# Performance work log

Hardware: AMD Instinct MI355X
Metric: run time of the kernel (lower is better)

The kernel has to match this reference:

```python
import jax, jax.numpy as jnp
import numpy as np
import math

SCALES = (1, 2, 4)
GROUPS = 8
EPS = 1e-5
TEMPERATURE = 1.0


def bilinear_resize(x, out_h, out_w):
    # torch F.interpolate mode='bilinear', align_corners=False
    B, C, h, w = x.shape
    def coords(out, in_):
        c = (jnp.arange(out, dtype=x.dtype) + 0.5) * (in_ / out) - 0.5
        c = jnp.clip(c, 0.0, in_ - 1.0)
        i0 = jnp.floor(c).astype(jnp.int32)
        i1 = jnp.minimum(i0 + 1, in_ - 1)
        t = c - i0.astype(x.dtype)
        return i0, i1, t
    y0, y1, ty = coords(out_h, h)
    x0, x1, tx = coords(out_w, w)
    r0 = x[:, :, y0, :]
    r1 = x[:, :, y1, :]
    v00 = r0[:, :, :, x0]; v01 = r0[:, :, :, x1]
    v10 = r1[:, :, :, x0]; v11 = r1[:, :, :, x1]
    top = v00 * (1.0 - tx) + v01 * tx
    bot = v10 * (1.0 - tx) + v11 * tx
    return top * (1.0 - ty)[:, None] + bot * ty[:, None]


def group_norm(x, gamma, beta):
    B, C, H, W = x.shape
    xg = x.reshape(B, GROUPS, C // GROUPS, H, W)
    mu = xg.mean(axis=(2, 3, 4), keepdims=True)
    var = xg.var(axis=(2, 3, 4), keepdims=True)
    xn = ((xg - mu) * jax.lax.rsqrt(var + EPS)).reshape(B, C, H, W)
    return xn * gamma[None, :, None, None] + beta[None, :, None, None]


def setup_inputs() -> dict:
    key = jax.random.key(0)
    B, C, H, W = 4, 128, 64, 64
    inter = max(C // 4, 8)  # 32
    S = len(SCALES)
    ks = jax.random.split(key, 8)
    def xavier(k, shape, fan_in, fan_out):
        a = math.sqrt(6.0 / (fan_in + fan_out))
        return jax.random.uniform(k, shape, jnp.float32, -a, a)
    inp = {
        'x': jax.random.normal(ks[0], (B, C, H, W), jnp.float32),
        'gn_w': jnp.ones((S, C), jnp.float32),
        'gn_b': jnp.zeros((S, C), jnp.float32),
        'qw': xavier(ks[1], (S, inter, C), C, inter),
        'qb': jnp.zeros((S, inter), jnp.float32),
        'kw': xavier(ks[2], (S, inter, C), C, inter),
        'kb': jnp.zeros((S, inter), jnp.float32),
        'vw': xavier(ks[3], (S, inter, C), C, inter),
        'vb': jnp.zeros((S, inter), jnp.float32),
        'ow': xavier(ks[4], (S, C, inter), inter, C),
        'ob': jnp.zeros((S, C), jnp.float32),
        'gamma': jnp.full((S,), 0.1 / S, jnp.float32),
        'scale_weights': jnp.full((S,), 1.0 / S, jnp.float32),
    }
    return inp


def _forward(x, gn_w, gn_b, qw, qb, kw, kb, vw, vb, ow, ob, gamma, scale_weights):
    B, C, H, W = x.shape
    inter = qw.shape[1]
    inv_scale = 1.0 / (TEMPERATURE * math.sqrt(inter))
    outs = []
    for i, s in enumerate(SCALES):
        if s == 1:
            xs = x
        else:
            xs = x.reshape(B, C, H // s, s, W // s, s).mean(axis=(3, 5))
        h, w = xs.shape[2], xs.shape[3]
        N = h * w
        xn = group_norm(xs, gn_w[i], gn_b[i])
        # 1x1 convs as channel contractions
        q = (jnp.einsum('oc,bchw->bohw', qw[i], xn) + qb[i][None, :, None, None]).reshape(B, inter, N)
        k = (jnp.einsum('oc,bchw->bohw', kw[i], xn) + kb[i][None, :, None, None]).reshape(B, inter, N)
        v = (jnp.einsum('oc,bchw->bohw', vw[i], xn) + vb[i][None, :, None, None]).reshape(B, inter, N)
        logits = jnp.einsum('bin,bim->bnm', q, k) * inv_scale  # [B, N, N]
        attn = jax.nn.softmax(logits, axis=-1)
        att = jnp.einsum('bnm,bim->bin', attn, v).reshape(B, inter, h, w)
        o = jnp.einsum('ci,bihw->bchw', ow[i], att) + ob[i][None, :, None, None]
        y = gamma[i] * o + xs
        if s > 1:
            y = bilinear_resize(y, H, W)
        outs.append(y)
    wts = jax.nn.softmax(scale_weights, axis=0)
    fused = wts[0] * outs[0]
    for i in range(1, len(outs)):
        fused = fused + wts[i] * outs[i]
    return fused


def reference(x, gn_w, gn_b, qw, qb, kw, kb, vw, vb, ow, ob, gamma, scale_weights):
    return _forward(x, gn_w, gn_b, qw, qb, kw, kb, vw, vb, ow, ob, gamma, scale_weights)
```

## Files before the change

kernel.cpp:

```cpp
#include <hip/hip_runtime.h>
#include <math.h>

#define B 4
#define C 128
#define CPG 16
#define INTER 32
#define SPLIT 16
#define KS1 8
#define KS24 4

#define N1 4096
#define N2 1024
#define N4 256

#define QOFF2 (B * N1 * 32)
#define QOFF4 (QOFF2 + B * N2 * 32)
#define QTOT  (QOFF4 + B * N4 * 32)
#define PAOFF2 (B * KS1 * 32 * N1)
#define PAOFF4 (PAOFF2 + B * KS24 * 32 * N2)
#define PATOT  (PAOFF4 + B * KS24 * 32 * N4)
#define PMOFF2 (B * KS1 * 2 * N1)
#define PMOFF4 (PMOFF2 + B * KS24 * 2 * N2)
#define PMTOT  (PMOFF4 + B * KS24 * 2 * N4)

#define QSCALE 0.25503490f

typedef unsigned short ushort_t;
typedef __attribute__((ext_vector_type(8))) short short8;
typedef __attribute__((ext_vector_type(4))) float f32x4;

__device__ __forceinline__ ushort_t f2bf(float f) {
    union { float f; unsigned u; } x; x.f = f;
    unsigned r = x.u + 0x7fffu + ((x.u >> 16) & 1u);
    return (ushort_t)(r >> 16);
}

__device__ __forceinline__ void scale_wts(const float* __restrict__ sw,
                                          float& w0, float& w1, float& w2) {
    float a = sw[0], b = sw[1], c = sw[2];
    float m = fmaxf(a, fmaxf(b, c));
    float e0 = __expf(a - m), e1 = __expf(b - m), e2 = __expf(c - m);
    float inv = 1.0f / (e0 + e1 + e2);
    w0 = e0 * inv; w1 = e1 * inv; w2 = e2 * inv;
}

__device__ __forceinline__ void block_reduce_write(float s, float q,
                                                   float* __restrict__ dst2) {
    __shared__ float rs[256], rq[256];
    rs[threadIdx.x] = s; rq[threadIdx.x] = q;
    __syncthreads();
    for (int st = 128; st > 0; st >>= 1) {
        if (threadIdx.x < st) {
            rs[threadIdx.x] += rs[threadIdx.x + st];
            rq[threadIdx.x] += rq[threadIdx.x + st];
        }
        __syncthreads();
    }
    if (threadIdx.x == 0) { dst2[0] = rs[0]; dst2[1] = rq[0]; }
}

__global__ __launch_bounds__(256) void pool_stats_kernel(const float* __restrict__ x,
                                                         float* __restrict__ xs2,
                                                         float* __restrict__ xs4,
                                                         float* __restrict__ part) {
    int bid = blockIdx.x;
    if (bid < 512) {
        int sp = bid & 15, bg = bid >> 4;
        const float* base = x + ((bg * CPG) << 12) + sp * 4096;
        float s = 0.0f, q = 0.0f;
        for (int i = threadIdx.x; i < 4096; i += 256) {
            float v = base[i];
            s += v; q += v * v;
        }
        block_reduce_write(s, q, part + bid * 2);
    } else if (bid < 1024) {
        int blk = bid - 512;
        int sp = blk & 15, bg = blk >> 4;
        int bc = bg * CPG + sp;
        const float* src = x + (bc << 12);
        float* dst = xs2 + (bc << 10);
        float s = 0.0f, q = 0.0f;
        for (int p = threadIdx.x; p < 1024; p += 256) {
            int oy = p >> 5, ox = p & 31;
            const float* s2 = src + oy * 128 + ox * 2;
            float v = (s2[0] + s2[1] + s2[64] + s2[65]) * 0.25f;
            dst[p] = v; s += v; q += v * v;
        }
        block_reduce_write(s, q, part + 1024 + blk * 2);
    } else {
        int blk = bid - 1024;
        int sp = blk & 15, bg = blk >> 4;
        int bc = bg * CPG + sp;
        const float* src = x + (bc << 12);
        float* dst = xs4 + (bc << 8);
        int p = threadIdx.x & 255;
        int oy = p >> 4, ox = p & 15;
        const float* s4 = src + oy * 256 + ox * 4;
        float v = 0.0f;
        #pragma unroll
        for (int dy = 0; dy < 4; ++dy)
            #pragma unroll
            for (int dx = 0; dx < 4; ++dx) v += s4[dy * 64 + dx];
        v *= 0.0625f;
        dst[p] = v;
        block_reduce_write(v, v * v, part + 2048 + blk * 2);
    }
}

template <int N, int NSH>
__device__ __forceinline__ void qkv_body(int bi, const float* __restrict__ xs,
    const float* __restrict__ part,
    const float* __restrict__ gn_w, const float* __restrict__ gn_b,
    const float* __restrict__ qw, const float* __restrict__ qb,
    const float* __restrict__ kw, const float* __restrict__ kb,
    const float* __restrict__ vw, const float* __restrict__ vb,
    ushort_t* __restrict__ q_bf, ushort_t* __restrict__ k_bf, ushort_t* __restrict__ v_bf) {
    const int nc = N >> 8;
    int nchunk = bi % nc; bi /= nc;
    int og = bi & 3; bi >>= 2;
    int proj = bi % 3; int b = bi / 3;
    const float* wp = (proj == 0) ? qw : ((proj == 1) ? kw : vw);
    const float* bp = (proj == 0) ? qb : ((proj == 1) ? kb : vb);
    __shared__ float wl[8 * 128];
    __shared__ float2 ss[128];
    {
        int t = threadIdx.x;
        #pragma unroll
        for (int r = 0; r < 4; ++r) {
            int e = r * 256 + t;
            int o = e >> 7, c0 = e & 127;
            wl[c0 * 8 + o] = wp[(og * 8 + o) * C + c0];
        }
        if (t < 128) {
            int c = t;
            int bg = b * 8 + (c >> 4);
            float s = 0.0f, q = 0.0f;
            #pragma unroll
            for (int sp = 0; sp < SPLIT; ++sp) {
                s += part[(bg * SPLIT + sp) * 2];
                q += part[(bg * SPLIT + sp) * 2 + 1];
            }
            float inv = 1.0f / (float)(CPG << NSH);
            float mu = s * inv;
            float var = q * inv - mu * mu;
            float a = rsqrtf(var + 1e-5f) * gn_w[c];
            float2 r; r.x = a; r.y = gn_b[c] - mu * a;
            ss[c] = r;
        }
    }
    __syncthreads();
    int n = nchunk * 256 + threadIdx.x;
    const float* xb = xs + ((size_t)(b * C) << NSH) + n;
    float acc[8];
    #pragma unroll
    for (int o = 0; o < 8; ++o) acc[o] = bp[og * 8 + o];
    #pragma unroll 2
    for (int c0 = 0; c0 < C; ++c0) {
        float raw = xb[(size_t)c0 << NSH];
        float2 s2 = ss[c0];
        float xv = fmaf(s2.x, raw, s2.y);
        const float4* wr = (const float4*)&wl[c0 * 8];
        float4 w0 = wr[0], w1 = wr[1];
        acc[0] += w0.x * xv; acc[1] += w0.y * xv; acc[2] += w0.z * xv; acc[3] += w0.w * xv;
        acc[4] += w1.x * xv; acc[5] += w1.y * xv; acc[6] += w1.z * xv; acc[7] += w1.w * xv;
    }
    if (proj < 2) {
        float fs = (proj == 0) ? QSCALE : 1.0f;
        ushort_t tmp[8];
        #pragma unroll
        for (int o = 0; o < 8; ++o) tmp[o] = f2bf(acc[o] * fs);
        ushort_t* dst = ((proj == 0) ? q_bf : k_bf) + ((size_t)(b * N + n)) * 32 + og * 8;
        *(uint4*)dst = *(const uint4*)tmp;
    } else {
        #pragma unroll
        for (int o = 0; o < 8; ++o)
            v_bf[((size_t)(b * 32 + og * 8 + o) << NSH) + n] = f2bf(acc[o]);
    }
}

__global__ __launch_bounds__(256) void qkv_all_kernel(const float* __restrict__ x,
    const float* __restrict__ xs2, const float* __restrict__ xs4,
    const float* __restrict__ part,
    const float* __restrict__ gn_w, const float* __restrict__ gn_b,
    const float* __restrict__ qw, const float* __restrict__ qb,
    const float* __restrict__ kw, const float* __restrict__ kb,
    const float* __restrict__ vw, const float* __restrict__ vb,
    ushort_t* __restrict__ qbf, ushort_t* __restrict__ kbf, ushort_t* __restrict__ vbf) {
    int bid = blockIdx.x;
    if (bid < 768) {
        qkv_body<N1, 12>(bid, x, part, gn_w, gn_b, qw, qb, kw, kb, vw, vb, qbf, kbf, vbf);
    } else if (bid < 960) {
        qkv_body<N2, 10>(bid - 768, xs2, part + 1024, gn_w + C, gn_b + C,
                         qw + INTER * C, qb + INTER, kw + INTER * C, kb + INTER,
                         vw + INTER * C, vb + INTER,
                         qbf + QOFF2, kbf + QOFF2, vbf + QOFF2);
    } else {
        qkv_body<N4, 8>(bid - 960, xs4, part + 2048, gn_w + 2 * C, gn_b + 2 * C,
                        qw + 2 * INTER * C, qb + 2 * INTER, kw + 2 * INTER * C, kb + 2 * INTER,
                        vw + 2 * INTER * C, vb + 2 * INTER,
                        qbf + QOFF4, kbf + QOFF4, vbf + QOFF4);
    }
}

#define SOFTMAX_PACK(sa, mrun, lrun, aA, aB, PwF)                                              \
    {                                                                                          \
        float s_[16];                                                                          \
        _Pragma("unroll")                                                                      \
        for (int kt = 0; kt < 4; ++kt) {                                                       \
            s_[kt * 4 + 0] = sa[kt][0]; s_[kt * 4 + 1] = sa[kt][1];                            \
            s_[kt * 4 + 2] = sa[kt][2]; s_[kt * 4 + 3] = sa[kt][3];                            \
        }                                                                                      \
        float t0 = fmaxf(fmaxf(s_[0], s_[1]), s_[2]);                                          \
        float t1 = fmaxf(fmaxf(s_[3], s_[4]), s_[5]);                                          \
        float t2 = fmaxf(fmaxf(s_[6], s_[7]), s_[8]);                                          \
        float t3 = fmaxf(fmaxf(s_[9], s_[10]), s_[11]);                                        \
        float t4 = fmaxf(fmaxf(s_[12], s_[13]), s_[14]);                                       \
        float tmax = fmaxf(fmaxf(fmaxf(t0, t1), fmaxf(t2, t3)), fmaxf(t4, s_[15]));            \
        tmax = fmaxf(tmax, __shfl_xor(tmax, 16, 64));                                          \
        tmax = fmaxf(tmax, __shfl_xor(tmax, 32, 64));                                          \
        if (!__all(tmax - mrun <= 8.0f)) {                                                     \
            float nmx = fmaxf(mrun, tmax);                                                     \
            float corr = exp2f(mrun - nmx);                                                    \
            lrun *= corr;                                                                      \
            _Pragma("unroll")                                                                  \
            for (int e = 0; e < 4; ++e) { aA[e] *= corr; aB[e] *= corr; }                       \
            mrun = nmx;                                                                        \
        }                                                                                      \
        float p_[16];                                                                          \
        float psum = 0.0f;                                                                     \
        _Pragma("unroll")                                                                      \
        for (int j = 0; j < 16; ++j) { p_[j] = exp2f(s_[j] - mrun); psum += p_[j]; }           \
        psum += __shfl_xor(psum, 16, 64);                                                      \
        psum += __shfl_xor(psum, 32, 64);                                                      \
        lrun += psum;                                                                          \
        _Pragma("unroll")                                                                      \
        for (int kt = 0; kt < 4; ++kt) {                                                       \
            unsigned u01, u23;                                                                 \
            asm("v_cvt_pk_bf16_f32 %0, %1, %2" : "=v"(u01) : "v"(p_[kt * 4 + 0]), "v"(p_[kt * 4 + 1])); \
            asm("v_cvt_pk_bf16_f32 %0, %1, %2" : "=v"(u23) : "v"(p_[kt * 4 + 2]), "v"(p_[kt * 4 + 3])); \
            uint2 pv; pv.x = u01; pv.y = u23;                                                  \
            *(uint2*)&(PwF)[lq * 64 + (((kt * 32 + g * 8) ^ ((lq & 7) << 4)) >> 1)] = pv;      \
        }                                                                                      \
    }

template <int N, int NSH, int KSL>
__device__ __forceinline__ void attn_body(int bi,
    const ushort_t* __restrict__ q_bf, const ushort_t* __restrict__ k_bf,
    const ushort_t* __restrict__ v_bf,
    float* __restrict__ pacc, float* __restrict__ pml,
    ushort_t* K_lds, ushort_t* V_lds, ushort_t* P_lds) {
    int ks = bi % KSL; bi /= KSL;
    const int nqc = N >> 7;
    int qc = bi % nqc; int b = bi / nqc;
    int tid = threadIdx.x;
    int l = tid & 63, w = tid >> 6, lq = l & 15, g = l >> 4;
    int q0 = qc * 128 + w * 32;

    short8 qf0 = *(const short8*)(q_bf + ((size_t)(b * N + q0 + lq)) * 32 + g * 8);
    short8 qf1 = *(const short8*)(q_bf + ((size_t)(b * N + q0 + 16 + lq)) * 32 + g * 8);
    f32x4 a00 = {0.f, 0.f, 0.f, 0.f}, a01 = {0.f, 0.f, 0.f, 0.f};
    f32x4 a10 = {0.f, 0.f, 0.f, 0.f}, a11 = {0.f, 0.f, 0.f, 0.f};
    float m0 = -3.0e38f, l0 = 0.0f, m1 = -3.0e38f, l1 = 0.0f;

    const int kchunk = N / KSL;
    int kbase = ks * kchunk;
    const int ntiles = kchunk >> 6;
    ushort_t* Pw = P_lds + w * (32 * 64);

    const int krow = tid >> 2;
    const int kidx = krow * 32 + ((((tid & 3) * 16) ^ ((krow & 3) << 4)) >> 1);
    const int vrow = tid >> 3;
    const int vidx = vrow * 64 + ((((tid & 7) * 16) ^ ((vrow & 7) << 4)) >> 1);

    const uint4* ksrc = (const uint4*)(k_bf + ((size_t)(b * N + kbase + krow)) * 32 + (tid & 3) * 8);
    const uint4* vsrc = (const uint4*)(v_bf + (((size_t)(b * 32 + vrow)) << NSH) + kbase + (tid & 7) * 8);
    uint4 kreg = *ksrc, vreg = *vsrc;

    const int ksw = (g ^ (lq & 3)) << 3;
    const int vsw0 = ((g * 16) ^ ((lq & 7) << 4)) >> 1;
    const int vsw1 = ((64 + g * 16) ^ ((lq & 7) << 4)) >> 1;

    for (int t = 0; t < ntiles; ++t) {
        __syncthreads();
        *(uint4*)&K_lds[kidx] = kreg;
        *(uint4*)&V_lds[vidx] = vreg;
        __syncthreads();
        if (t + 1 < ntiles) {
            ksrc += 256; vsrc += 8;
            kreg = *ksrc; vreg = *vsrc;
        }

        f32x4 sa0[4], sa1[4];
        #pragma unroll
        for (int kt = 0; kt < 4; ++kt) {
            short8 kf = *(const short8*)&K_lds[(kt * 16 + lq) * 32 + ksw];
            f32x4 z = {0.f, 0.f, 0.f, 0.f};
            sa0[kt] = __builtin_amdgcn_mfma_f32_16x16x32_bf16(kf, qf0, z, 0, 0, 0);
            sa1[kt] = __builtin_amdgcn_mfma_f32_16x16x32_bf16(kf, qf1, z, 0, 0, 0);
        }
        SOFTMAX_PACK(sa0, m0, l0, a00, a01, Pw)
        SOFTMAX_PACK(sa1, m1, l1, a10, a11, (Pw + 16 * 64))

        short8 vf00 = *(const short8*)&V_lds[lq * 64 + vsw0];
        short8 vf10 = *(const short8*)&V_lds[(16 + lq) * 64 + vsw0];
        short8 vf01 = *(const short8*)&V_lds[lq * 64 + vsw1];
        short8 vf11 = *(const short8*)&V_lds[(16 + lq) * 64 + vsw1];
        short8 p00 = *(const short8*)&Pw[lq * 64 + vsw0];
        short8 p01 = *(const short8*)&Pw[lq * 64 + vsw1];
        short8 p10 = *(const short8*)&Pw[(16 + lq) * 64 + vsw0];
        short8 p11 = *(const short8*)&Pw[(16 + lq) * 64 + vsw1];
        a00 = __builtin_amdgcn_mfma_f32_16x16x32_bf16(vf00, p00, a00, 0, 0, 0);
        a01 = __builtin_amdgcn_mfma_f32_16x16x32_bf16(vf10, p00, a01, 0, 0, 0);
        a00 = __builtin_amdgcn_mfma_f32_16x16x32_bf16(vf01, p01, a00, 0, 0, 0);
        a01 = __builtin_amdgcn_mfma_f32_16x16x32_bf16(vf11, p01, a01, 0, 0, 0);
        a10 = __builtin_amdgcn_mfma_f32_16x16x32_bf16(vf00, p10, a10, 0, 0, 0);
        a11 = __builtin_amdgcn_mfma_f32_16x16x32_bf16(vf10, p10, a11, 0, 0, 0);
        a10 = __builtin_amdgcn_mfma_f32_16x16x32_bf16(vf01, p11, a10, 0, 0, 0);
        a11 = __builtin_amdgcn_mfma_f32_16x16x32_bf16(vf11, p11, a11, 0, 0, 0);
    }
    int n0 = q0 + lq, n1 = q0 + 16 + lq;
    size_t pb_ = ((size_t)(b * KSL + ks)) * 32;
    #pragma unroll
    for (int r = 0; r < 4; ++r) {
        pacc[(pb_ + (g * 4 + r)) * N + n0]      = a00[r];
        pacc[(pb_ + 16 + (g * 4 + r)) * N + n0] = a01[r];
        pacc[(pb_ + (g * 4 + r)) * N + n1]      = a10[r];
        pacc[(pb_ + 16 + (g * 4 + r)) * N + n1] = a11[r];
    }
    if (g == 0) {
        pml[((size_t)(b * KSL + ks) * 2) * N + n0]     = m0;
        pml[((size_t)(b * KSL + ks) * 2 + 1) * N + n0] = l0;
        pml[((size_t)(b * KSL + ks) * 2) * N + n1]     = m1;
        pml[((size_t)(b * KSL + ks) * 2 + 1) * N + n1] = l1;
    }
}

__global__ __launch_bounds__(256) void attn_all_kernel(
    const ushort_t* __restrict__ qbf, const ushort_t* __restrict__ kbf,
    const ushort_t* __restrict__ vbf,
    float* __restrict__ pacc, float* __restrict__ pml) {
    __shared__ ushort_t K_lds[64 * 32];
    __shared__ ushort_t V_lds[32 * 64];
    __shared__ ushort_t P_lds[4 * 32 * 64];
    int bid = blockIdx.x;
    if (bid < 1024) {
        attn_body<N1, 12, KS1>(bid, qbf, kbf, vbf, pacc, pml, K_lds, V_lds, P_lds);
    } else if (bid < 1152) {
        attn_body<N2, 10, KS24>(bid - 1024, qbf + QOFF2, kbf + QOFF2, vbf + QOFF2,
                                pacc + PAOFF2, pml + PMOFF2, K_lds, V_lds, P_lds);
    } else {
        attn_body<N4, 8, KS24>(bid - 1152, qbf + QOFF4, kbf + QOFF4, vbf + QOFF4,
                               pacc + PAOFF4, pml + PMOFF4, K_lds, V_lds, P_lds);
    }
}

template <int N, int NSH, int KSL>
__device__ __forceinline__ void comb_oy_body(int tile, const float* __restrict__ pacc,
    const float* __restrict__ pml, const float* __restrict__ ow, const float* __restrict__ ob,
    const float* __restrict__ gamma, const float* __restrict__ xs,
    float* __restrict__ ydst, const float* __restrict__ sw,
    float* att_lds, float* ow_lds) {
    const int ntiles = N >> 5;
    int b = tile / ntiles;
    int n0 = (tile % ntiles) << 5;
    int t = threadIdx.x;
    {
        const float4* src = (const float4*)ow;
        float4* dst = (float4*)ow_lds;
        dst[t] = src[t]; dst[256 + t] = src[256 + t];
        dst[512 + t] = src[512 + t]; dst[768 + t] = src[768 + t];
    }
    {
        int o = t >> 3, j = t & 7;
        int n = n0 + j * 4;
        float4 mv[KSL];
        float4 M = {-3.0e38f, -3.0e38f, -3.0e38f, -3.0e38f};
        #pragma unroll
        for (int k2 = 0; k2 < KSL; ++k2) {
            mv[k2] = *(const float4*)&pml[((size_t)(b * KSL + k2) * 2) * N + n];
            M.x = fmaxf(M.x, mv[k2].x); M.y = fmaxf(M.y, mv[k2].y);
            M.z = fmaxf(M.z, mv[k2].z); M.w = fmaxf(M.w, mv[k2].w);
        }
        float4 L = {0.f, 0.f, 0.f, 0.f}, A = {0.f, 0.f, 0.f, 0.f};
        #pragma unroll
        for (int k2 = 0; k2 < KSL; ++k2) {
            float4 lv = *(const float4*)&pml[((size_t)(b * KSL + k2) * 2 + 1) * N + n];
            float4 av = *(const float4*)&pacc[((size_t)(b * KSL + k2) * INTER + o) * N + n];
            float4 wg;
            wg.x = exp2f(mv[k2].x - M.x); wg.y = exp2f(mv[k2].y - M.y);
            wg.z = exp2f(mv[k2].z - M.z); wg.w = exp2f(mv[k2].w - M.w);
            L.x += lv.x * wg.x; L.y += lv.y * wg.y;
            L.z += lv.z * wg.z; L.w += lv.w * wg.w;
            A.x += av.x * wg.x; A.y += av.y * wg.y;
            A.z += av.z * wg.z; A.w += av.w * wg.w;
        }
        float4 r;
        r.x = A.x / L.x; r.y = A.y / L.y; r.z = A.z / L.z; r.w = A.w / L.w;
        *(float4*)&att_lds[o * 36 + j * 4] = r;
    }
    __syncthreads();
    {
        int n = t & 31, cg2 = t >> 5;
        float av[32];
        #pragma unroll
        for (int i = 0; i < 32; ++i) av[i] = att_lds[i * 36 + n];
        float gm = gamma[0];
        float wsc = 1.0f;
        if (sw) { float w0, w1, w2; scale_wts(sw, w0, w1, w2); wsc = w0; }
        const float* xsb = xs + ((size_t)(b * C + cg2 * 16) << NSH) + n0 + n;
        float* yb = ydst + ((size_t)(b * C + cg2 * 16) << NSH) + n0 + n;
        #pragma unroll 4
        for (int cc = 0; cc < 16; ++cc) {
            int c = cg2 * 16 + cc;
            const float4* wr = (const float4*)&ow_lds[c * 32];
            float a0 = 0.f, a1 = 0.f, a2 = 0.f, a3 = 0.f;
            #pragma unroll
            for (int i4 = 0; i4 < 8; ++i4) {
                float4 wv = wr[i4];
                a0 += wv.x * av[i4 * 4 + 0]; a1 += wv.y * av[i4 * 4 + 1];
                a2 += wv.z * av[i4 * 4 + 2]; a3 += wv.w * av[i4 * 4 + 3];
            }
            float o_ = ob[c] + ((a0 + a1) + (a2 + a3));
            float y = gm * o_ + xsb[(size_t)cc << NSH];
            yb[(size_t)cc << NSH] = wsc * y;
        }
    }
    __syncthreads();
}

__global__ __launch_bounds__(256) void comb_oy_all_kernel(const float* __restrict__ pacc,
    const float* __restrict__ pml,
    const float* __restrict__ ow, const float* __restrict__ ob,
    const float* __restrict__ gamma,
    const float* __restrict__ x, const float* __restrict__ xs2, const float* __restrict__ xs4,
    float* __restrict__ out, float* __restrict__ y2, float* __restrict__ y4,
    const float* __restrict__ sw) {
    __shared__ float att_lds[32 * 36];
    __shared__ float ow_lds[128 * 32];
    int bid = blockIdx.x;
    if (bid < 512) {
        comb_oy_body<N1, 12, KS1>(bid, pacc, pml, ow, ob, gamma, x, out, sw, att_lds, ow_lds);
    } else if (bid < 640) {
        comb_oy_body<N2, 10, KS24>(bid - 512, pacc + PAOFF2, pml + PMOFF2,
                                   ow + C * INTER, ob + C, gamma + 1, xs2, y2, nullptr,
                                   att_lds, ow_lds);
    } else {
        comb_oy_body<N4, 8, KS24>(bid - 640, pacc + PAOFF4, pml + PMOFF4,
                                  ow + 2 * C * INTER, ob + 2 * C, gamma + 2, xs4, y4, nullptr,
                                  att_lds, ow_lds);
    }
}

__device__ __forceinline__ float bilerp(const float* __restrict__ img, int in,
                                        int oy, int ox, float r) {
    float cy = (oy + 0.5f) * r - 0.5f;
    cy = fminf(fmaxf(cy, 0.0f), (float)(in - 1));
    float cx = (ox + 0.5f) * r - 0.5f;
    cx = fminf(fmaxf(cx, 0.0f), (float)(in - 1));
    int y0 = (int)cy; int y1i = (y0 + 1 < in) ? y0 + 1 : in - 1; float ty = cy - (float)y0;
    int x0 = (int)cx; int x1i = (x0 + 1 < in) ? x0 + 1 : in - 1; float tx = cx - (float)x0;
    float v00 = img[y0 * in + x0];
    float v01 = img[y0 * in + x1i];
    float v10 = img[y1i * in + x0];
    float v11 = img[y1i * in + x1i];
    float top = v00 * (1.0f - tx) + v01 * tx;
    float bot = v10 * (1.0f - tx) + v11 * tx;
    return top * (1.0f - ty) + bot * ty;
}

__global__ __launch_bounds__(256) void fuse_kernel(float* __restrict__ out,
                                                   const float* __restrict__ y2,
                                                   const float* __restrict__ y4,
                                                   const float* __restrict__ sw) {
    int idx = blockIdx.x * 256 + threadIdx.x;
    int p = idx & 4095;
    int bc = idx >> 12;
    int oy = p >> 6, ox = p & 63;
    float w0, w1, w2; scale_wts(sw, w0, w1, w2);
    float v2 = bilerp(y2 + bc * 1024, 32, oy, ox, 0.5f);
    float v4 = bilerp(y4 + bc * 256, 16, oy, ox, 0.25f);
    out[idx] = out[idx] + w1 * v2 + w2 * v4;
}

extern "C" void kernel_launch(void* const* d_in, const int* in_sizes, int n_in,
                              void* d_out, int out_size, void* d_ws, size_t ws_size,
                              hipStream_t stream) {
    const float* x     = (const float*)d_in[0];
    const float* gn_w  = (const float*)d_in[1];
    const float* gn_b  = (const float*)d_in[2];
    const float* qw    = (const float*)d_in[3];
    const float* qb    = (const float*)d_in[4];
    const float* kw    = (const float*)d_in[5];
    const float* kb    = (const float*)d_in[6];
    const float* vw    = (const float*)d_in[7];
    const float* vb    = (const float*)d_in[8];
    const float* ow    = (const float*)d_in[9];
    const float* ob    = (const float*)d_in[10];
    const float* gamma = (const float*)d_in[11];
    const float* sw    = (const float*)d_in[12];
    float* out = (float*)d_out;

    float* ws    = (float*)d_ws;
    float* xs2   = ws;
    float* xs4   = xs2 + 524288;
    float* y2    = xs4 + 131072;
    float* y4    = y2 + 524288;
    float* part  = y4 + 131072;
    float* pacc  = part + 3072;
    float* pml   = pacc + PATOT;
    ushort_t* qbf = (ushort_t*)(pml + PMTOT);
    ushort_t* kbf = qbf + QTOT;
    ushort_t* vbf = kbf + QTOT;

    pool_stats_kernel<<<1536, 256, 0, stream>>>(x, xs2, xs4, part);
    qkv_all_kernel<<<1008, 256, 0, stream>>>(x, xs2, xs4, part, gn_w, gn_b,
                                             qw, qb, kw, kb, vw, vb, qbf, kbf, vbf);
    attn_all_kernel<<<1184, 256, 0, stream>>>(qbf, kbf, vbf, pacc, pml);
    comb_oy_all_kernel<<<672, 256, 0, stream>>>(pacc, pml, ow, ob, gamma,
                                                x, xs2, xs4, out, y2, y4, sw);
    fuse_kernel<<<8192, 256, 0, stream>>>(out, y2, y4, sw);
}
```

Measured before the change: 85.25 us.

## Restructure pipeline: fuse pooling stats per channel, widen QKV blocks, fuse resize into scale-1 combine

Pooling and group-norm statistics now come from one block per channel, and the three scale reductions are written into a six-value slot per channel. The QKV projection computes all 32 outputs per block, so fewer blocks each read the input once. The key-split count for scale 1 drops from 8 to 4. The standalone fuse kernel is removed: the scale 2/4 combine runs first, then the scale-1 combine does the bilinear upsampling and weighted sum directly, which avoids a round trip of the output through global memory. The tradeoffs are fewer blocks for QKV (252) and attention, more registers per thread, and one extra kernel launch ordering dependency.

Result: slower. 104.7 us (+22.9%).

```diff
diff --git a/kernel.cpp b/kernel.cpp
--- a/kernel.cpp
+++ b/kernel.cpp
@@ -5,9 +5,7 @@
 #define C 128
 #define CPG 16
 #define INTER 32
-#define SPLIT 16
-#define KS1 8
-#define KS24 4
+#define KS 4
 
 #define N1 4096
 #define N2 1024
@@ -16,12 +14,12 @@
 #define QOFF2 (B * N1 * 32)
 #define QOFF4 (QOFF2 + B * N2 * 32)
 #define QTOT  (QOFF4 + B * N4 * 32)
-#define PAOFF2 (B * KS1 * 32 * N1)
-#define PAOFF4 (PAOFF2 + B * KS24 * 32 * N2)
-#define PATOT  (PAOFF4 + B * KS24 * 32 * N4)
-#define PMOFF2 (B * KS1 * 2 * N1)
-#define PMOFF4 (PMOFF2 + B * KS24 * 2 * N2)
-#define PMTOT  (PMOFF4 + B * KS24 * 2 * N4)
+#define PAOFF2 (B * KS * 32 * N1)
+#define PAOFF4 (PAOFF2 + B * KS * 32 * N2)
+#define PATOT  (PAOFF4 + B * KS * 32 * N4)
+#define PMOFF2 (B * KS * 2 * N1)
+#define PMOFF4 (PMOFF2 + B * KS * 2 * N2)
+#define PMTOT  (PMOFF4 + B * KS * 2 * N4)
 
 #define QSCALE 0.25503490f
 
@@ -47,6 +45,7 @@
 __device__ __forceinline__ void block_reduce_write(float s, float q,
                                                    float* __restrict__ dst2) {
     __shared__ float rs[256], rq[256];
+    __syncthreads();
     rs[threadIdx.x] = s; rq[threadIdx.x] = q;
     __syncthreads();
     for (int st = 128; st > 0; st >>= 1) {
@@ -63,118 +62,102 @@
                                                          float* __restrict__ xs2,
                                                          float* __restrict__ xs4,
                                                          float* __restrict__ part) {
-    int bid = blockIdx.x;
-    if (bid < 512) {
-        int sp = bid & 15, bg = bid >> 4;
-        const float* base = x + ((bg * CPG) << 12) + sp * 4096;
-        float s = 0.0f, q = 0.0f;
-        for (int i = threadIdx.x; i < 4096; i += 256) {
-            float v = base[i];
-            s += v; q += v * v;
-        }
-        block_reduce_write(s, q, part + bid * 2);
-    } else if (bid < 1024) {
-        int blk = bid - 512;
-        int sp = blk & 15, bg = blk >> 4;
-        int bc = bg * CPG + sp;
-        const float* src = x + (bc << 12);
-        float* dst = xs2 + (bc << 10);
-        float s = 0.0f, q = 0.0f;
-        for (int p = threadIdx.x; p < 1024; p += 256) {
-            int oy = p >> 5, ox = p & 31;
-            const float* s2 = src + oy * 128 + ox * 2;
-            float v = (s2[0] + s2[1] + s2[64] + s2[65]) * 0.25f;
-            dst[p] = v; s += v; q += v * v;
-        }
-        block_reduce_write(s, q, part + 1024 + blk * 2);
-    } else {
-        int blk = bid - 1024;
-        int sp = blk & 15, bg = blk >> 4;
-        int bc = bg * CPG + sp;
-        const float* src = x + (bc << 12);
-        float* dst = xs4 + (bc << 8);
-        int p = threadIdx.x & 255;
-        int oy = p >> 4, ox = p & 15;
-        const float* s4 = src + oy * 256 + ox * 4;
+    int bc = blockIdx.x;
+    const float* src = x + ((size_t)bc << 12);
+    int t = threadIdx.x;
+    float s1 = 0.0f, q1 = 0.0f;
+    for (int i = t; i < 4096; i += 256) {
+        float v = src[i];
+        s1 += v; q1 += v * v;
+    }
+    float* dst2 = xs2 + ((size_t)bc << 10);
+    float s2 = 0.0f, q2 = 0.0f;
+    for (int p = t; p < 1024; p += 256) {
+        int oy = p >> 5, ox = p & 31;
+        const float* sp = src + oy * 128 + ox * 2;
+        float v = (sp[0] + sp[1] + sp[64] + sp[65]) * 0.25f;
+        dst2[p] = v; s2 += v; q2 += v * v;
+    }
+    float* dst4 = xs4 + ((size_t)bc << 8);
+    float s4 = 0.0f, q4 = 0.0f;
+    {
+        int oy = t >> 4, ox = t & 15;
+        const float* sp = src + oy * 256 + ox * 4;
         float v = 0.0f;
         #pragma unroll
         for (int dy = 0; dy < 4; ++dy)
             #pragma unroll
-            for (int dx = 0; dx < 4; ++dx) v += s4[dy * 64 + dx];
+            for (int dx = 0; dx < 4; ++dx) v += sp[dy * 64 + dx];
         v *= 0.0625f;
-        dst[p] = v;
-        block_reduce_write(v, v * v, part + 2048 + blk * 2);
-    }
-}
-
-template <int N, int NSH>
-__device__ __forceinline__ void qkv_body(int bi, const float* __restrict__ xs,
-    const float* __restrict__ part,
+        dst4[t] = v; s4 = v; q4 = v * v;
+    }
+    block_reduce_write(s1, q1, part + bc * 6);
+    block_reduce_write(s2, q2, part + bc * 6 + 2);
+    block_reduce_write(s4, q4, part + bc * 6 + 4);
+}
+
+template <int N, int NSH, int SLOT>
+__device__ __forceinline__ void qkv_body(int proj, int b, int nchunk,
+    const float* __restrict__ xs, const float* __restrict__ part,
     const float* __restrict__ gn_w, const float* __restrict__ gn_b,
-    const float* __restrict__ qw, const float* __restrict__ qb,
-    const float* __restrict__ kw, const float* __restrict__ kb,
-    const float* __restrict__ vw, const float* __restrict__ vb,
+    const float* __restrict__ wp, const float* __restrict__ bp,
     ushort_t* __restrict__ q_bf, ushort_t* __restrict__ k_bf, ushort_t* __restrict__ v_bf) {
-    const int nc = N >> 8;
-    int nchunk = bi % nc; bi /= nc;
-    int og = bi & 3; bi >>= 2;
-    int proj = bi % 3; int b = bi / 3;
-    const float* wp = (proj == 0) ? qw : ((proj == 1) ? kw : vw);
-    const float* bp = (proj == 0) ? qb : ((proj == 1) ? kb : vb);
-    __shared__ float wl[8 * 128];
+    __shared__ float wl[128 * 32];
     __shared__ float2 ss[128];
-    {
-        int t = threadIdx.x;
-        #pragma unroll
-        for (int r = 0; r < 4; ++r) {
-            int e = r * 256 + t;
-            int o = e >> 7, c0 = e & 127;
-            wl[c0 * 8 + o] = wp[(og * 8 + o) * C + c0];
-        }
-        if (t < 128) {
-            int c = t;
-            int bg = b * 8 + (c >> 4);
-            float s = 0.0f, q = 0.0f;
-            #pragma unroll
-            for (int sp = 0; sp < SPLIT; ++sp) {
-                s += part[(bg * SPLIT + sp) * 2];
-                q += part[(bg * SPLIT + sp) * 2 + 1];
-            }
-            float inv = 1.0f / (float)(CPG << NSH);
-            float mu = s * inv;
-            float var = q * inv - mu * mu;
-            float a = rsqrtf(var + 1e-5f) * gn_w[c];
-            float2 r; r.x = a; r.y = gn_b[c] - mu * a;
-            ss[c] = r;
-        }
+    int t = threadIdx.x;
+    #pragma unroll
+    for (int r = 0; r < 16; ++r) {
+        int e = r * 256 + t;
+        int c0 = e >> 5, o = e & 31;
+        wl[e] = wp[o * C + c0];
+    }
+    if (t < 128) {
+        int c = t;
+        int gbase = b * C + ((c >> 4) << 4);
+        float s = 0.0f, q = 0.0f;
+        #pragma unroll
+        for (int j = 0; j < 16; ++j) {
+            s += part[(gbase + j) * 6 + SLOT * 2];
+            q += part[(gbase + j) * 6 + SLOT * 2 + 1];
+        }
+        float inv = 1.0f / (float)(CPG << NSH);
+        float mu = s * inv;
+        float var = q * inv - mu * mu;
+        float a = rsqrtf(var + 1e-5f) * gn_w[c];
+        float2 r; r.x = a; r.y = gn_b[c] - mu * a;
+        ss[c] = r;
     }
     __syncthreads();
-    int n = nchunk * 256 + threadIdx.x;
+    int n = nchunk * 256 + t;
     const float* xb = xs + ((size_t)(b * C) << NSH) + n;
-    float acc[8];
+    float acc[32];
     #pragma unroll
-    for (int o = 0; o < 8; ++o) acc[o] = bp[og * 8 + o];
+    for (int o = 0; o < 32; ++o) acc[o] = bp[o];
     #pragma unroll 2
     for (int c0 = 0; c0 < C; ++c0) {
-        float raw = xb[(size_t)c0 << NSH];
         float2 s2 = ss[c0];
-        float xv = fmaf(s2.x, raw, s2.y);
-        const float4* wr = (const float4*)&wl[c0 * 8];
-        float4 w0 = wr[0], w1 = wr[1];
-        acc[0] += w0.x * xv; acc[1] += w0.y * xv; acc[2] += w0.z * xv; acc[3] += w0.w * xv;
-        acc[4] += w1.x * xv; acc[5] += w1.y * xv; acc[6] += w1.z * xv; acc[7] += w1.w * xv;
+        float xv = fmaf(s2.x, xb[(size_t)c0 << NSH], s2.y);
+        const float4* wr = (const float4*)&wl[c0 * 32];
+        #pragma unroll
+        for (int i4 = 0; i4 < 8; ++i4) {
+            float4 wv = wr[i4];
+            acc[i4 * 4 + 0] += wv.x * xv; acc[i4 * 4 + 1] += wv.y * xv;
+            acc[i4 * 4 + 2] += wv.z * xv; acc[i4 * 4 + 3] += wv.w * xv;
+        }
     }
     if (proj < 2) {
         float fs = (proj == 0) ? QSCALE : 1.0f;
-        ushort_t tmp[8];
-        #pragma unroll
-        for (int o = 0; o < 8; ++o) tmp[o] = f2bf(acc[o] * fs);
-        ushort_t* dst = ((proj == 0) ? q_bf : k_bf) + ((size_t)(b * N + n)) * 32 + og * 8;
-        *(uint4*)dst = *(const uint4*)tmp;
+        ushort_t tmp[32];
+        #pragma unroll
+        for (int o = 0; o < 32; ++o) tmp[o] = f2bf(acc[o] * fs);
+        ushort_t* dst = ((proj == 0) ? q_bf : k_bf) + (size_t)(b * N + n) * 32;
+        const uint4* tv = (const uint4*)tmp;
+        ((uint4*)dst)[0] = tv[0]; ((uint4*)dst)[1] = tv[1];
+        ((uint4*)dst)[2] = tv[2]; ((uint4*)dst)[3] = tv[3];
     } else {
         #pragma unroll
-        for (int o = 0; o < 8; ++o)
-            v_bf[((size_t)(b * 32 + og * 8 + o) << NSH) + n] = f2bf(acc[o]);
+        for (int o = 0; o < 32; ++o)
+            v_bf[((size_t)(b * 32 + o) << NSH) + n] = f2bf(acc[o]);
     }
 }
 
@@ -187,18 +170,25 @@
     const float* __restrict__ vw, const float* __restrict__ vb,
     ushort_t* __restrict__ qbf, ushort_t* __restrict__ kbf, ushort_t* __restrict__ vbf) {
     int bid = blockIdx.x;
-    if (bid < 768) {
-        qkv_body<N1, 12>(bid, x, part, gn_w, gn_b, qw, qb, kw, kb, vw, vb, qbf, kbf, vbf);
-    } else if (bid < 960) {
-        qkv_body<N2, 10>(bid - 768, xs2, part + 1024, gn_w + C, gn_b + C,
-                         qw + INTER * C, qb + INTER, kw + INTER * C, kb + INTER,
-                         vw + INTER * C, vb + INTER,
-                         qbf + QOFF2, kbf + QOFF2, vbf + QOFF2);
+    if (bid < 192) {
+        int proj = bid / 64, r = bid % 64, b_ = r >> 4, nch = r & 15;
+        const float* wp = (proj == 0) ? qw : ((proj == 1) ? kw : vw);
+        const float* bp = (proj == 0) ? qb : ((proj == 1) ? kb : vb);
+        qkv_body<N1, 12, 0>(proj, b_, nch, x, part, gn_w, gn_b, wp, bp, qbf, kbf, vbf);
+    } else if (bid < 240) {
+        int u = bid - 192;
+        int proj = u / 16, r = u % 16, b_ = r >> 2, nch = r & 3;
+        const float* wp = ((proj == 0) ? qw : ((proj == 1) ? kw : vw)) + INTER * C;
+        const float* bp = ((proj == 0) ? qb : ((proj == 1) ? kb : vb)) + INTER;
+        qkv_body<N2, 10, 1>(proj, b_, nch, xs2, part, gn_w + C, gn_b + C, wp, bp,
+                            qbf + QOFF2, kbf + QOFF2, vbf + QOFF2);
     } else {
-        qkv_body<N4, 8>(bid - 960, xs4, part + 2048, gn_w + 2 * C, gn_b + 2 * C,
-                        qw + 2 * INTER * C, qb + 2 * INTER, kw + 2 * INTER * C, kb + 2 * INTER,
-                        vw + 2 * INTER * C, vb + 2 * INTER,
-                        qbf + QOFF4, kbf + QOFF4, vbf + QOFF4);
+        int u = bid - 240;
+        int proj = u / 4, b_ = u % 4;
+        const float* wp = ((proj == 0) ? qw : ((proj == 1) ? kw : vw)) + 2 * INTER * C;
+        const float* bp = ((proj == 0) ? qb : ((proj == 1) ? kb : vb)) + 2 * INTER;
+        qkv_body<N4, 8, 2>(proj, b_, 0, xs4, part, gn_w + 2 * C, gn_b + 2 * C, wp, bp,
+                           qbf + QOFF4, kbf + QOFF4, vbf + QOFF4);
     }
 }
 
@@ -243,13 +233,13 @@
         }                                                                                      \
     }
 
-template <int N, int NSH, int KSL>
+template <int N, int NSH>
 __device__ __forceinline__ void attn_body(int bi,
     const ushort_t* __restrict__ q_bf, const ushort_t* __restrict__ k_bf,
     const ushort_t* __restrict__ v_bf,
     float* __restrict__ pacc, float* __restrict__ pml,
     ushort_t* K_lds, ushort_t* V_lds, ushort_t* P_lds) {
-    int ks = bi % KSL; bi /= KSL;
+    int ks = bi % KS; bi /= KS;
     const int nqc = N >> 7;
     int qc = bi % nqc; int b = bi / nqc;
     int tid = threadIdx.x;
@@ -262,7 +252,7 @@
     f32x4 a10 = {0.f, 0.f, 0.f, 0.f}, a11 = {0.f, 0.f, 0.f, 0.f};
     float m0 = -3.0e38f, l0 = 0.0f, m1 = -3.0e38f, l1 = 0.0f;
 
-    const int kchunk = N / KSL;
+    const int kchunk = N / KS;
     int kbase = ks * kchunk;
     const int ntiles = kchunk >> 6;
     ushort_t* Pw = P_lds + w * (32 * 64);
@@ -319,7 +309,7 @@
         a11 = __builtin_amdgcn_mfma_f32_16x16x32_bf16(vf11, p11, a11, 0, 0, 0);
     }
     int n0 = q0 + lq, n1 = q0 + 16 + lq;
-    size_t pb_ = ((size_t)(b * KSL + ks)) * 32;
+    size_t pb_ = ((size_t)(b * KS + ks)) * 32;
     #pragma unroll
     for (int r = 0; r < 4; ++r) {
         pacc[(pb_ + (g * 4 + r)) * N + n0]      = a00[r];
@@ -328,10 +318,10 @@
         pacc[(pb_ + 16 + (g * 4 + r)) * N + n1] = a11[r];
     }
     if (g == 0) {
-        pml[((size_t)(b * KSL + ks) * 2) * N + n0]     = m0;
-        pml[((size_t)(b * KSL + ks) * 2 + 1) * N + n0] = l0;
-        pml[((size_t)(b * KSL + ks) * 2) * N + n1]     = m1;
-        pml[((size_t)(b * KSL + ks) * 2 + 1) * N + n1] = l1;
+        pml[((size_t)(b * KS + ks) * 2) * N + n0]     = m0;
+        pml[((size_t)(b * KS + ks) * 2 + 1) * N + n0] = l0;
+        pml[((size_t)(b * KS + ks) * 2) * N + n1]     = m1;
+        pml[((size_t)(b * KS + ks) * 2 + 1) * N + n1] = l1;
     }
 }
 
@@ -343,23 +333,22 @@
     __shared__ ushort_t V_lds[32 * 64];
     __shared__ ushort_t P_lds[4 * 32 * 64];
     int bid = blockIdx.x;
-    if (bid < 1024) {
-        attn_body<N1, 12, KS1>(bid, qbf, kbf, vbf, pacc, pml, K_lds, V_lds, P_lds);
-    } else if (bid < 1152) {
-        attn_body<N2, 10, KS24>(bid - 1024, qbf + QOFF2, kbf + QOFF2, vbf + QOFF2,
-                                pacc + PAOFF2, pml + PMOFF2, K_lds, V_lds, P_lds);
+    if (bid < 512) {
+        attn_body<N1, 12>(bid, qbf, kbf, vbf, pacc, pml, K_lds, V_lds, P_lds);
+    } else if (bid < 640) {
+        attn_body<N2, 10>(bid - 512, qbf + QOFF2, kbf + QOFF2, vbf + QOFF2,
+                          pacc + PAOFF2, pml + PMOFF2, K_lds, V_lds, P_lds);
     } else {
-        attn_body<N4, 8, KS24>(bid - 1152, qbf + QOFF4, kbf + QOFF4, vbf + QOFF4,
-                               pacc + PAOFF4, pml + PMOFF4, K_lds, V_lds, P_lds);
-    }
-}
-
-template <int N, int NSH, int KSL>
+        attn_body<N4, 8>(bid - 640, qbf + QOFF4, kbf + QOFF4, vbf + QOFF4,
+                         pacc + PAOFF4, pml + PMOFF4, K_lds, V_lds, P_lds);
+    }
+}
+
+template <int N, int NSH>
 __device__ __forceinline__ void comb_oy_body(int tile, const float* __restrict__ pacc,
     const float* __restrict__ pml, const float* __restrict__ ow, const float* __restrict__ ob,
     const float* __restrict__ gamma, const float* __restrict__ xs,
-    float* __restrict__ ydst, const float* __restrict__ sw,
-    float* att_lds, float* ow_lds) {
+    float* __restrict__ ydst, float* att_lds, float* ow_lds) {
     const int ntiles = N >> 5;
     int b = tile / ntiles;
     int n0 = (tile % ntiles) << 5;
@@ -373,19 +362,19 @@
     {
         int o = t >> 3, j = t & 7;
         int n = n0 + j * 4;
-        float4 mv[KSL];
+        float4 mv[KS];
         float4 M = {-3.0e38f, -3.0e38f, -3.0e38f, -3.0e38f};
         #pragma unroll
-        for (int k2 = 0; k2 < KSL; ++k2) {
-            mv[k2] = *(const float4*)&pml[((size_t)(b * KSL + k2) * 2) * N + n];
+        for (int k2 = 0; k2 < KS; ++k2) {
+            mv[k2] = *(const float4*)&pml[((size_t)(b * KS + k2) * 2) * N + n];
             M.x = fmaxf(M.x, mv[k2].x); M.y = fmaxf(M.y, mv[k2].y);
             M.z = fmaxf(M.z, mv[k2].z); M.w = fmaxf(M.w, mv[k2].w);
         }
         float4 L = {0.f, 0.f, 0.f, 0.f}, A = {0.f, 0.f, 0.f, 0.f};
         #pragma unroll
-        for (int k2 = 0; k2 < KSL; ++k2) {
-            float4 lv = *(const float4*)&pml[((size_t)(b * KSL + k2) * 2 + 1) * N + n];
-            float4 av = *(const float4*)&pacc[((size_t)(b * KSL + k2) * INTER + o) * N + n];
+        for (int k2 = 0; k2 < KS; ++k2) {
+            float4 lv = *(const float4*)&pml[((size_t)(b * KS + k2) * 2 + 1) * N + n];
+            float4 av = *(const float4*)&pacc[((size_t)(b * KS + k2) * INTER + o) * N + n];
             float4 wg;
             wg.x = exp2f(mv[k2].x - M.x); wg.y = exp2f(mv[k2].y - M.y);
             wg.z = exp2f(mv[k2].z - M.z); wg.w = exp2f(mv[k2].w - M.w);
@@ -405,8 +394,6 @@
         #pragma unroll
         for (int i = 0; i < 32; ++i) av[i] = att_lds[i * 36 + n];
         float gm = gamma[0];
-        float wsc = 1.0f;
-        if (sw) { float w0, w1, w2; scale_wts(sw, w0, w1, w2); wsc = w0; }
         const float* xsb = xs + ((size_t)(b * C + cg2 * 16) << NSH) + n0 + n;
         float* yb = ydst + ((size_t)(b * C + cg2 * 16) << NSH) + n0 + n;
         #pragma unroll 4
@@ -421,65 +408,122 @@
                 a2 += wv.z * av[i4 * 4 + 2]; a3 += wv.w * av[i4 * 4 + 3];
             }
             float o_ = ob[c] + ((a0 + a1) + (a2 + a3));
-            float y = gm * o_ + xsb[(size_t)cc << NSH];
-            yb[(size_t)cc << NSH] = wsc * y;
-        }
-    }
-    __syncthreads();
-}
-
-__global__ __launch_bounds__(256) void comb_oy_all_kernel(const float* __restrict__ pacc,
+            yb[(size_t)cc << NSH] = gm * o_ + xsb[(size_t)cc << NSH];
+        }
+    }
+}
+
+__global__ __launch_bounds__(256) void comb_s24_kernel(const float* __restrict__ pacc,
     const float* __restrict__ pml,
     const float* __restrict__ ow, const float* __restrict__ ob,
     const float* __restrict__ gamma,
-    const float* __restrict__ x, const float* __restrict__ xs2, const float* __restrict__ xs4,
-    float* __restrict__ out, float* __restrict__ y2, float* __restrict__ y4,
-    const float* __restrict__ sw) {
+    const float* __restrict__ xs2, const float* __restrict__ xs4,
+    float* __restrict__ y2, float* __restrict__ y4) {
     __shared__ float att_lds[32 * 36];
     __shared__ float ow_lds[128 * 32];
     int bid = blockIdx.x;
-    if (bid < 512) {
-        comb_oy_body<N1, 12, KS1>(bid, pacc, pml, ow, ob, gamma, x, out, sw, att_lds, ow_lds);
-    } else if (bid < 640) {
-        comb_oy_body<N2, 10, KS24>(bid - 512, pacc + PAOFF2, pml + PMOFF2,
-                                   ow + C * INTER, ob + C, gamma + 1, xs2, y2, nullptr,
-                                   att_lds, ow_lds);
+    if (bid < 128) {
+        comb_oy_body<N2, 10>(bid, pacc + PAOFF2, pml + PMOFF2,
+                             ow + C * INTER, ob + C, gamma + 1, xs2, y2, att_lds, ow_lds);
     } else {
-        comb_oy_body<N4, 8, KS24>(bid - 640, pacc + PAOFF4, pml + PMOFF4,
-                                  ow + 2 * C * INTER, ob + 2 * C, gamma + 2, xs4, y4, nullptr,
-                                  att_lds, ow_lds);
-    }
-}
-
-__device__ __forceinline__ float bilerp(const float* __restrict__ img, int in,
-                                        int oy, int ox, float r) {
-    float cy = (oy + 0.5f) * r - 0.5f;
-    cy = fminf(fmaxf(cy, 0.0f), (float)(in - 1));
-    float cx = (ox + 0.5f) * r - 0.5f;
-    cx = fminf(fmaxf(cx, 0.0f), (float)(in - 1));
-    int y0 = (int)cy; int y1i = (y0 + 1 < in) ? y0 + 1 : in - 1; float ty = cy - (float)y0;
-    int x0 = (int)cx; int x1i = (x0 + 1 < in) ? x0 + 1 : in - 1; float tx = cx - (float)x0;
-    float v00 = img[y0 * in + x0];
-    float v01 = img[y0 * in + x1i];
-    float v10 = img[y1i * in + x0];
-    float v11 = img[y1i * in + x1i];
-    float top = v00 * (1.0f - tx) + v01 * tx;
-    float bot = v10 * (1.0f - tx) + v11 * tx;
-    return top * (1.0f - ty) + bot * ty;
-}
-
-__global__ __launch_bounds__(256) void fuse_kernel(float* __restrict__ out,
-                                                   const float* __restrict__ y2,
-                                                   const float* __restrict__ y4,
-                                                   const float* __restrict__ sw) {
-    int idx = blockIdx.x * 256 + threadIdx.x;
-    int p = idx & 4095;
-    int bc = idx >> 12;
-    int oy = p >> 6, ox = p & 63;
-    float w0, w1, w2; scale_wts(sw, w0, w1, w2);
-    float v2 = bilerp(y2 + bc * 1024, 32, oy, ox, 0.5f);
-    float v4 = bilerp(y4 + bc * 256, 16, oy, ox, 0.25f);
-    out[idx] = out[idx] + w1 * v2 + w2 * v4;
+        comb_oy_body<N4, 8>(bid - 128, pacc + PAOFF4, pml + PMOFF4,
+                            ow + 2 * C * INTER, ob + 2 * C, gamma + 2, xs4, y4,
+                            att_lds, ow_lds);
+    }
+}
+
+__global__ __launch_bounds__(256) void comb_oy_s1_fuse_kernel(
+    const float* __restrict__ pacc, const float* __restrict__ pml,
+    const float* __restrict__ ow, const float* __restrict__ ob,
+    const float* __restrict__ gamma, const float* __restrict__ x,
+    const float* __restrict__ y2, const float* __restrict__ y4,
+    float* __restrict__ out, const float* __restrict__ sw) {
+    __shared__ float att_lds[32 * 36];
+    __shared__ float ow_lds[128 * 32];
+    const int N = N1;
+    int tile = blockIdx.x;
+    int b = tile >> 7;
+    int n0 = (tile & 127) << 5;
+    int t = threadIdx.x;
+    {
+        const float4* src = (const float4*)ow;
+        float4* dst = (float4*)ow_lds;
+        dst[t] = src[t]; dst[256 + t] = src[256 + t];
+        dst[512 + t] = src[512 + t]; dst[768 + t] = src[768 + t];
+    }
+    {
+        int o = t >> 3, j = t & 7;
+        int n = n0 + j * 4;
+        float4 mv[KS];
+        float4 M = {-3.0e38f, -3.0e38f, -3.0e38f, -3.0e38f};
+        #pragma unroll
+        for (int k2 = 0; k2 < KS; ++k2) {
+            mv[k2] = *(const float4*)&pml[((size_t)(b * KS + k2) * 2) * N + n];
+            M.x = fmaxf(M.x, mv[k2].x); M.y = fmaxf(M.y, mv[k2].y);
+            M.z = fmaxf(M.z, mv[k2].z); M.w = fmaxf(M.w, mv[k2].w);
+        }
+        float4 L = {0.f, 0.f, 0.f, 0.f}, A = {0.f, 0.f, 0.f, 0.f};
+        #pragma unroll
+        for (int k2 = 0; k2 < KS; ++k2) {
+            float4 lv = *(const float4*)&pml[((size_t)(b * KS + k2) * 2 + 1) * N + n];
+            float4 av = *(const float4*)&pacc[((size_t)(b * KS + k2) * INTER + o) * N + n];
+            float4 wg;
+            wg.x = exp2f(mv[k2].x - M.x); wg.y = exp2f(mv[k2].y - M.y);
+            wg.z = exp2f(mv[k2].z - M.z); wg.w = exp2f(mv[k2].w - M.w);
+            L.x += lv.x * wg.x; L.y += lv.y * wg.y;
+            L.z += lv.z * wg.z; L.w += lv.w * wg.w;
+            A.x += av.x * wg.x; A.y += av.y * wg.y;
+            A.z += av.z * wg.z; A.w += av.w * wg.w;
+        }
+        float4 r;
+        r.x = A.x / L.x; r.y = A.y / L.y; r.z = A.z / L.z; r.w = A.w / L.w;
+        *(float4*)&att_lds[o * 36 + j * 4] = r;
+    }
+    __syncthreads();
+    {
+        int n = t & 31, cg2 = t >> 5;
+        float av[32];
+        #pragma unroll
+        for (int i = 0; i < 32; ++i) av[i] = att_lds[i * 36 + n];
+        float gm = gamma[0];
+        float w0, w1, w2; scale_wts(sw, w0, w1, w2);
+        int p = n0 + n, oy = p >> 6, ox = p & 63;
+        float cy2 = fminf(fmaxf((oy + 0.5f) * 0.5f - 0.5f, 0.0f), 31.0f);
+        int ya0 = (int)cy2; int ya1 = (ya0 + 1 < 32) ? ya0 + 1 : 31; float ty2 = cy2 - (float)ya0;
+        float cx2 = fminf(fmaxf((ox + 0.5f) * 0.5f - 0.5f, 0.0f), 31.0f);
+        int xa0 = (int)cx2; int xa1 = (xa0 + 1 < 32) ? xa0 + 1 : 31; float tx2 = cx2 - (float)xa0;
+        float cy4 = fminf(fmaxf((oy + 0.5f) * 0.25f - 0.5f, 0.0f), 15.0f);
+        int yb0 = (int)cy4; int yb1 = (yb0 + 1 < 16) ? yb0 + 1 : 15; float ty4 = cy4 - (float)yb0;
+        float cx4 = fminf(fmaxf((ox + 0.5f) * 0.25f - 0.5f, 0.0f), 15.0f);
+        int xb0 = (int)cx4; int xb1 = (xb0 + 1 < 16) ? xb0 + 1 : 15; float tx4 = cx4 - (float)xb0;
+        const float* xsb = x + ((size_t)(b * C + cg2 * 16) << 12) + p;
+        float* outp = out + ((size_t)(b * C + cg2 * 16) << 12) + p;
+        const float* y2b = y2 + (size_t)(b * C + cg2 * 16) * 1024;
+        const float* y4b = y4 + (size_t)(b * C + cg2 * 16) * 256;
+        #pragma unroll 4
+        for (int cc = 0; cc < 16; ++cc) {
+            int c = cg2 * 16 + cc;
+            const float4* wr = (const float4*)&ow_lds[c * 32];
+            float a0 = 0.f, a1 = 0.f, a2 = 0.f, a3 = 0.f;
+            #pragma unroll
+            for (int i4 = 0; i4 < 8; ++i4) {
+                float4 wv = wr[i4];
+                a0 += wv.x * av[i4 * 4 + 0]; a1 += wv.y * av[i4 * 4 + 1];
+                a2 += wv.z * av[i4 * 4 + 2]; a3 += wv.w * av[i4 * 4 + 3];
+            }
+            float o_ = ob[c] + ((a0 + a1) + (a2 + a3));
+            float yv = gm * o_ + xsb[(size_t)cc << 12];
+            const float* i2 = y2b + cc * 1024;
+            float top2 = i2[ya0 * 32 + xa0] * (1.f - tx2) + i2[ya0 * 32 + xa1] * tx2;
+            float bot2 = i2[ya1 * 32 + xa0] * (1.f - tx2) + i2[ya1 * 32 + xa1] * tx2;
+            float v2 = top2 * (1.f - ty2) + bot2 * ty2;
+            const float* i4p = y4b + cc * 256;
+            float top4 = i4p[yb0 * 16 + xb0] * (1.f - tx4) + i4p[yb0 * 16 + xb1] * tx4;
+            float bot4 = i4p[yb1 * 16 + xb0] * (1.f - tx4) + i4p[yb1 * 16 + xb1] * tx4;
+            float v4 = top4 * (1.f - ty4) + bot4 * ty4;
+            outp[(size_t)cc << 12] = w0 * yv + w1 * v2 + w2 * v4;
+        }
+    }
 }
 
 extern "C" void kernel_launch(void* const* d_in, const int* in_sizes, int n_in,
@@ -512,11 +556,12 @@
     ushort_t* kbf = qbf + QTOT;
     ushort_t* vbf = kbf + QTOT;
 
-    pool_stats_kernel<<<1536, 256, 0, stream>>>(x, xs2, xs4, part);
-    qkv_all_kernel<<<1008, 256, 0, stream>>>(x, xs2, xs4, part, gn_w, gn_b,
-                                             qw, qb, kw, kb, vw, vb, qbf, kbf, vbf);
-    attn_all_kernel<<<1184, 256, 0, stream>>>(qbf, kbf, vbf, pacc, pml);
-    comb_oy_all_kernel<<<672, 256, 0, stream>>>(pacc, pml, ow, ob, gamma,
-                                                x, xs2, xs4, out, y2, y4, sw);
-    fuse_kernel<<<8192, 256, 0, stream>>>(out, y2, y4, sw);
-}
+    pool_stats_kernel<<<512, 256, 0, stream>>>(x, xs2, xs4, part);
+    qkv_all_kernel<<<252, 256, 0, stream>>>(x, xs2, xs4, part, gn_w, gn_b,
+                                            qw, qb, kw, kb, vw, vb, qbf, kbf, vbf);
+    attn_all_kernel<<<672, 256, 0, stream>>>(qbf, kbf, vbf, pacc, pml);
+    comb_s24_kernel<<<160, 256, 0, stream>>>(pacc, pml, ow, ob, gamma,
+                                             xs2, xs4, y2, y4);
+    comb_oy_s1_fuse_kernel<<<512, 256, 0, stream>>>(pacc, pml, ow, ob, gamma,
+                                                    x, y2, y4, out, sw);
+}
```
